# Performance work log

Measured on AMD Instinct MI355X. Metric: run time of the kernel, lower is better.

## Reference

```python
import jax, jax.numpy as jnp
import numpy as np

B, T, C = 8, 1024, 1024
NH, HD = 16, 64          # num_heads, head_dim (C = NH*HD)
NL = 8                   # num_layers
TPB = 64                 # tokens_per_block (block_causal)
EPS = 1e-5


def setup_inputs() -> dict:
    key = jax.random.key(0)
    ks = jax.random.split(key, 12)
    s = 0.02
    sequences = jax.random.normal(ks[0], (B, T, C), dtype=jnp.float32)
    # block-causal mask: causal OR same-block (tril | block_diag)
    idx = jnp.arange(T)
    mask = (idx[:, None] >= idx[None, :]) | ((idx[:, None] // TPB) == (idx[None, :] // TPB))
    # stacked per-layer params; torch Linear convention: W has shape [out, in]
    d = {
        "sequences": sequences,
        "mask": mask,
        "Wq": jax.random.normal(ks[1], (NL, C, C)) * s, "bq": jnp.zeros((NL, C)),
        "Wk": jax.random.normal(ks[2], (NL, C, C)) * s, "bk": jnp.zeros((NL, C)),
        "Wv": jax.random.normal(ks[3], (NL, C, C)) * s, "bv": jnp.zeros((NL, C)),
        "Wo": jax.random.normal(ks[4], (NL, C, C)) * s, "bo": jnp.zeros((NL, C)),
        "ln1w": jnp.ones((NL, C)), "ln1b": jnp.zeros((NL, C)),
        "ln2w": jnp.ones((NL, C)), "ln2b": jnp.zeros((NL, C)),
        "W1": jax.random.normal(ks[5], (NL, 4 * C, C)) * s, "b1": jnp.zeros((NL, 4 * C)),
        "W2": jax.random.normal(ks[6], (NL, C, 4 * C)) * s, "b2": jnp.zeros((NL, C)),
        "lnfw": jnp.ones((C,)), "lnfb": jnp.zeros((C,)),
    }
    return d


def _layernorm(x, w, b):
    m = jnp.mean(x, axis=-1, keepdims=True)
    v = jnp.mean(jnp.square(x - m), axis=-1, keepdims=True)
    return (x - m) * jax.lax.rsqrt(v + EPS) * w + b


def _linear(x, W, b):  # x: [..., in], W: [out, in]
    return jnp.einsum('...i,oi->...o', x, W) + b


def _attention(h, mask, Wq, bq, Wk, bk, Wv, bv, Wo, bo):
    # h: [B,T,C]
    q = _linear(h, Wq, bq).reshape(B, T, NH, HD)
    k = _linear(h, Wk, bk).reshape(B, T, NH, HD)
    v = _linear(h, Wv, bv).reshape(B, T, NH, HD)
    att = jnp.einsum('bqhd,bkhd->bhqk', q, k) * (HD ** -0.5)
    att = jnp.where(mask, att, -jnp.inf)
    att = jax.nn.softmax(att, axis=-1)
    y = jnp.einsum('bhqk,bkhd->bqhd', att, v).reshape(B, T, C)
    return _linear(y, Wo, bo)


def reference(sequences, mask, Wq, bq, Wk, bk, Wv, bv, Wo, bo,
              ln1w, ln1b, ln2w, ln2b, W1, b1, W2, b2, lnfw, lnfb):
    x = sequences  # dropout p=0
    for i in range(NL):
        h = _layernorm(x, ln1w[i], ln1b[i])
        x = x + _attention(h, mask, Wq[i], bq[i], Wk[i], bk[i], Wv[i], bv[i], Wo[i], bo[i])
        h = _layernorm(x, ln2w[i], ln2b[i])
        h = _linear(h, W1[i], b1[i])
        h = jax.nn.gelu(h, approximate=False)  # torch nn.GELU default = exact erf
        x = x + _linear(h, W2[i], b2[i])
    return _layernorm(x, lnfw, lnfb)
```

## Files before the change

### kernel.cpp

```cpp
#include <hip/hip_runtime.h>
#include <math.h>

typedef unsigned short ushort_t;
typedef __attribute__((ext_vector_type(4))) float f32x4;
typedef __attribute__((ext_vector_type(8))) short short8;

constexpr int BATCH = 8, T = 1024, C = 1024, NH = 16, HD = 64, NL = 8;
constexpr int MROWS = BATCH * T;
constexpr int CS = 3 * C;

#define WAITVM(n) asm volatile("s_waitcnt vmcnt(" #n ")" ::: "memory")
#define WAITLGKM0 asm volatile("s_waitcnt lgkmcnt(0)" ::: "memory")

__device__ __forceinline__ ushort_t f2bf(float f) {
  unsigned u = __builtin_bit_cast(unsigned, f);
  u += 0x7fffu + ((u >> 16) & 1u);
  return (ushort_t)(u >> 16);
}

__device__ __forceinline__ void gload_lds16(const ushort_t* g, ushort_t* l) {
  __builtin_amdgcn_global_load_lds(
      (const __attribute__((address_space(1))) unsigned int*)g,
      (__attribute__((address_space(3))) unsigned int*)l, 16, 0, 0);
}

__global__ __launch_bounds__(256, 8)
void convw_kernel(const float* __restrict__ Wq, const float* __restrict__ Wk,
                  const float* __restrict__ Wv, const float* __restrict__ Wo,
                  const float* __restrict__ W1, const float* __restrict__ W2,
                  const float* __restrict__ bq, const float* __restrict__ bk,
                  const float* __restrict__ bv,
                  ushort_t* __restrict__ wqkv, ushort_t* __restrict__ wo,
                  ushort_t* __restrict__ w1, ushort_t* __restrict__ w2,
                  float* __restrict__ bqkv)
{
  if (blockIdx.x == 6144) {
    int t = threadIdx.x;
    if (t < 384) {
      const float* s = (t < 128) ? (bq + t * 8)
                     : (t < 256) ? (bk + (t - 128) * 8)
                                 : (bv + (t - 256) * 8);
      f32x4 a = ((const f32x4*)s)[0], b = ((const f32x4*)s)[1];
      ((f32x4*)(bqkv + t * 8))[0] = a;
      ((f32x4*)(bqkv + t * 8))[1] = b;
    }
    return;
  }
  int g = blockIdx.x * 256 + threadIdx.x;
  const float* src;
  ushort_t* dst;
  if (g < 393216) {
    int which = g >> 17;
    int r = g & 131071;
    src = (which == 0 ? Wq : which == 1 ? Wk : Wv) + (size_t)r * 8;
    dst = wqkv + (size_t)g * 8;
  } else if (g < 524288) {
    int r = g - 393216;
    src = Wo + (size_t)r * 8; dst = wo + (size_t)r * 8;
  } else if (g < 1048576) {
    int r = g - 524288;
    src = W1 + (size_t)r * 8; dst = w1 + (size_t)r * 8;
  } else {
    int r = g - 1048576;
    src = W2 + (size_t)r * 8; dst = w2 + (size_t)r * 8;
  }
  f32x4 a = ((const f32x4*)src)[0], b = ((const f32x4*)src)[1];
  short8 o;
#pragma unroll
  for (int e = 0; e < 4; ++e) { o[e] = (short)f2bf(a[e]); o[e + 4] = (short)f2bf(b[e]); }
  *(short8*)dst = o;
}

template<int MODE>
__global__ __launch_bounds__(256, 4)
void gemm97(const ushort_t* __restrict__ A, const ushort_t* __restrict__ Wb,
            const float* __restrict__ bias, ushort_t* __restrict__ outb,
            float* __restrict__ resid, int K, int N, int nbn)
{
  __shared__ __align__(16) ushort_t Sm[2 * 128 * 64];
  ushort_t* As = Sm;
  ushort_t* Bs = Sm + 128 * 64;

  const int tid = threadIdx.x;
  const int lane = tid & 63, wave = tid >> 6;
  const int wm = wave >> 1, wn = wave & 1;
  const int l15 = lane & 15, l4 = lane >> 4;

  const int xcd = blockIdx.x & 7;
  const int local = blockIdx.x >> 3;
  const int grp = local >> 5, rem = local & 31;
  const int bm = xcd * 8 + (rem >> 2);
  const int bn = grp * 4 + (rem & 3);
  const long bm0 = (long)bm * 128;
  const long bn0 = (long)bn * 128;

  const ushort_t* srcA[4]; const ushort_t* srcB[4]; int dst4[4];
#pragma unroll
  for (int j = 0; j < 4; ++j) {
    int cidx = j * 256 + tid;
    int row = cidx >> 3;
    int cl = (cidx & 7) ^ (row & 7);
    srcA[j] = A + (size_t)(bm0 + row) * K + cl * 8;
    srcB[j] = Wb + (size_t)(bn0 + row) * K + cl * 8;
    dst4[j] = cidx * 8;
  }
  int aoff[2][4], boff[2][4];
#pragma unroll
  for (int ks = 0; ks < 2; ++ks) {
#pragma unroll
    for (int i = 0; i < 4; ++i) {
      int ra = wm * 64 + i * 16 + l15;
      aoff[ks][i] = ra * 64 + (((ks * 4 + l4) ^ (ra & 7)) << 3);
      int rb = wn * 64 + i * 16 + l15;
      boff[ks][i] = rb * 64 + (((ks * 4 + l4) ^ (rb & 7)) << 3);
    }
  }

  f32x4 acc[4][4] = {};
  const int nt = K >> 6;

  for (int t = 0; t < nt; ++t) {
    __syncthreads();
    const int kt = t << 6;
#pragma unroll
    for (int j = 0; j < 4; ++j) {
      gload_lds16(srcA[j] + kt, &As[dst4[j]]);
      gload_lds16(srcB[j] + kt, &Bs[dst4[j]]);
    }
    __syncthreads();
#pragma unroll
    for (int ks = 0; ks < 2; ++ks) {
      short8 af[4], bfr[4];
#pragma unroll
      for (int i = 0; i < 4; ++i) {
        af[i] = *(const short8*)&As[aoff[ks][i]];
        bfr[i] = *(const short8*)&Bs[boff[ks][i]];
      }
#pragma unroll
      for (int mi = 0; mi < 4; ++mi)
#pragma unroll
        for (int ni = 0; ni < 4; ++ni)
          acc[mi][ni] = __builtin_amdgcn_mfma_f32_16x16x32_bf16(
              af[mi], bfr[ni], acc[mi][ni], 0, 0, 0);
    }
  }
  __syncthreads();

  float* fl = (float*)Sm + wave * (16 * 68);
  const long grow0 = bm0 + wm * 64;
  const long gcol0 = bn0 + wn * 64;
  const int c8 = lane & 7;
  const f32x4 bb0 = *(const f32x4*)&bias[gcol0 + c8 * 8];
  const f32x4 bb1 = *(const f32x4*)&bias[gcol0 + c8 * 8 + 4];

#pragma unroll
  for (int mi = 0; mi < 4; ++mi) {
#pragma unroll
    for (int ni = 0; ni < 4; ++ni)
#pragma unroll
      for (int r = 0; r < 4; ++r)
        fl[(l4 * 4 + r) * 68 + ni * 16 + l15] = acc[mi][ni][r];
#pragma unroll
    for (int pass = 0; pass < 2; ++pass) {
      int row = pass * 8 + (lane >> 3);
      f32x4 v0 = *(const f32x4*)&fl[row * 68 + c8 * 8];
      f32x4 v1 = *(const f32x4*)&fl[row * 68 + c8 * 8 + 4];
      v0 += bb0; v1 += bb1;
      const long grow = grow0 + mi * 16 + row;
      if (MODE == 1) {
#pragma unroll
        for (int e = 0; e < 4; ++e) {
          v0[e] = 0.5f * v0[e] * (1.0f + erff(v0[e] * 0.70710678118f));
          v1[e] = 0.5f * v1[e] * (1.0f + erff(v1[e] * 0.70710678118f));
        }
      }
      if (MODE == 2) {
        float* rp = resid + (size_t)grow * N + gcol0 + c8 * 8;
        f32x4 r0 = *(const f32x4*)rp;
        f32x4 r1 = *(const f32x4*)(rp + 4);
        r0 += v0; r1 += v1;
        *(f32x4*)rp = r0;
        *(f32x4*)(rp + 4) = r1;
      } else {
        short8 o;
#pragma unroll
        for (int e = 0; e < 4; ++e) { o[e] = (short)f2bf(v0[e]); o[e + 4] = (short)f2bf(v1[e]); }
        *(short8*)&outb[(size_t)grow * N + gcol0 + c8 * 8] = o;
      }
    }
  }
}

__global__ __launch_bounds__(256, 4)
void attn_kernel(const ushort_t* __restrict__ qkv, ushort_t* __restrict__ y)
{
  __shared__ __align__(16) ushort_t Ks[2][64 * 64];
  __shared__ __align__(16) ushort_t Vts[2][64 * 64];
  __shared__ __align__(16) ushort_t Ps[64 * 64];
  const int tid = threadIdx.x;
  const int lane = tid & 63, wave = tid >> 6;
  const int l15 = lane & 15, l4 = lane >> 4;
  const int w16 = wave * 16;
  const int bh = blockIdx.x & 127, qpair = blockIdx.x >> 7;
  const int h = bh & 15, b = bh >> 4;
  const int qoff = h * HD, koff = C + h * HD, voff = 2 * C + h * HD;
  const int kvr = tid & 63, dc = tid >> 6;

#pragma unroll
  for (int half = 0; half < 2; ++half) {
    const int qb = half == 0 ? qpair : 15 - qpair;
    const int nkv = qb + 1;
    const size_t qrow0 = (size_t)(b * T + qb * 64);

    short8 aq[2];
#pragma unroll
    for (int ks = 0; ks < 2; ++ks)
      aq[ks] = *(const short8*)(qkv + (qrow0 + w16 + l15) * CS + qoff + ks * 32 + l4 * 8);

    f32x4 o[4] = {};
    float mrun[4] = {-INFINITY, -INFINITY, -INFINITY, -INFINITY};
    float lrun[4] = {0.f, 0.f, 0.f, 0.f};

    {
      const size_t krow0 = (size_t)(b * T);
#pragma unroll
      for (int j = 0; j < 2; ++j) {
        int cidx = j * 256 + tid;
        int row = cidx >> 3, cl = (cidx & 7) ^ (row & 7);
        gload_lds16(qkv + (krow0 + row) * CS + koff + cl * 8, &Ks[0][cidx * 8]);
      }
    }
    short8 vreg0, vreg1;
    vreg0 = *(const short8*)(qkv + ((size_t)(b * T) + kvr) * CS + voff + dc * 8);
    vreg1 = *(const short8*)(qkv + ((size_t)(b * T) + kvr) * CS + voff + (dc + 4) * 8);
    WAITVM(2);
    __builtin_amdgcn_s_barrier();

    for (int t = 0; t < nkv; ++t) {
      const int buf = t & 1;
      const bool more = (t + 1 < nkv);
      short8 vnext0, vnext1;
      if (more) {
        const size_t krow1 = (size_t)(b * T + (t + 1) * 64);
#pragma unroll
        for (int j = 0; j < 2; ++j) {
          int cidx = j * 256 + tid;
          int row = cidx >> 3, cl = (cidx & 7) ^ (row & 7);
          gload_lds16(qkv + (krow1 + row) * CS + koff + cl * 8, &Ks[buf ^ 1][cidx * 8]);
        }
        vnext0 = *(const short8*)(qkv + (krow1 + kvr) * CS + voff + dc * 8);
        vnext1 = *(const short8*)(qkv + (krow1 + kvr) * CS + voff + (dc + 4) * 8);
      }

      f32x4 s[4] = {};
#pragma unroll
      for (int ks = 0; ks < 2; ++ks) {
#pragma unroll
        for (int n = 0; n < 4; ++n) {
          int br = n * 16 + l15;
          int pb = (ks * 4 + l4) ^ (br & 7);
          short8 bk2 = *(const short8*)&Ks[buf][br * 64 + pb * 8];
          s[n] = __builtin_amdgcn_mfma_f32_16x16x32_bf16(aq[ks], bk2, s[n], 0, 0, 0);
        }
      }

#pragma unroll
      for (int r = 0; r < 4; ++r) {
        float mx = fmaxf(fmaxf(s[0][r], s[1][r]), fmaxf(s[2][r], s[3][r]));
#pragma unroll
        for (int d = 1; d < 16; d <<= 1) mx = fmaxf(mx, __shfl_xor(mx, d, 16));
        mx *= 0.125f;
        float mnew = fmaxf(mrun[r], mx);
        float alpha = __expf(mrun[r] - mnew);
        float rowsum = 0.f;
        int qr = w16 + l4 * 4 + r;
#pragma unroll
        for (int n = 0; n < 4; ++n) {
          float pv = __expf(s[n][r] * 0.125f - mnew);
          rowsum += pv;
          int kv = n * 16 + l15;
          Ps[qr * 64 + (((kv >> 3) ^ (qr & 7)) << 3) + (kv & 7)] = f2bf(pv);
        }
#pragma unroll
        for (int d = 1; d < 16; d <<= 1) rowsum += __shfl_xor(rowsum, d, 16);
        mrun[r] = mnew;
        lrun[r] = lrun[r] * alpha + rowsum;
        o[0][r] *= alpha; o[1][r] *= alpha; o[2][r] *= alpha; o[3][r] *= alpha;
      }

#pragma unroll
      for (int i = 0; i < 8; ++i) {
        int d0 = dc * 8 + i;
        Vts[buf][d0 * 64 + (((kvr >> 3) ^ (d0 & 7)) << 3) + (kvr & 7)] = (ushort_t)vreg0[i];
        int d1 = (dc + 4) * 8 + i;
        Vts[buf][d1 * 64 + (((kvr >> 3) ^ (d1 & 7)) << 3) + (kvr & 7)] = (ushort_t)vreg1[i];
      }
      vreg0 = vnext0; vreg1 = vnext1;

      WAITLGKM0;
      __builtin_amdgcn_s_barrier();

#pragma unroll
      for (int ks = 0; ks < 2; ++ks) {
        int arow = w16 + l15;
        int pa = (ks * 4 + l4) ^ (arow & 7);
        short8 ap = *(const short8*)&Ps[arow * 64 + pa * 8];
#pragma unroll
        for (int n = 0; n < 4; ++n) {
          int vr = n * 16 + l15;
          int pb = (ks * 4 + l4) ^ (vr & 7);
          short8 bvv = *(const short8*)&Vts[buf][vr * 64 + pb * 8];
          o[n] = __builtin_amdgcn_mfma_f32_16x16x32_bf16(ap, bvv, o[n], 0, 0, 0);
        }
      }

      if (more) { WAITVM(2); }
      __builtin_amdgcn_s_barrier();
    }

#pragma unroll
    for (int n = 0; n < 4; ++n) {
#pragma unroll
      for (int r = 0; r < 4; ++r) {
        float val = o[n][r] / lrun[r];
        y[(qrow0 + w16 + l4 * 4 + r) * C + h * HD + n * 16 + l15] = f2bf(val);
      }
    }
    __builtin_amdgcn_s_barrier();
  }
}

template<int OUTBF16>
__global__ __launch_bounds__(256, 4)
void ln_kernel(const float* __restrict__ x, const float* __restrict__ w,
               const float* __restrict__ bprm, void* __restrict__ out)
{
  const size_t row = blockIdx.x;
  const int tid = threadIdx.x;
  f32x4 xv = ((const f32x4*)(x + row * 1024))[tid];
  float s1 = xv[0] + xv[1] + xv[2] + xv[3];
  float s2 = xv[0] * xv[0] + xv[1] * xv[1] + xv[2] * xv[2] + xv[3] * xv[3];
#pragma unroll
  for (int m = 1; m < 64; m <<= 1) {
    s1 += __shfl_xor(s1, m);
    s2 += __shfl_xor(s2, m);
  }
  __shared__ float red[8];
  const int wave = tid >> 6, lane = tid & 63;
  if (lane == 0) { red[wave * 2] = s1; red[wave * 2 + 1] = s2; }
  __syncthreads();
  s1 = red[0] + red[2] + red[4] + red[6];
  s2 = red[1] + red[3] + red[5] + red[7];
  const float mean = s1 * (1.f / 1024.f);
  const float var = s2 * (1.f / 1024.f) - mean * mean;
  const float rstd = rsqrtf(var + 1e-5f);
  f32x4 wv = ((const f32x4*)w)[tid];
  f32x4 bv = ((const f32x4*)bprm)[tid];
  f32x4 ov;
#pragma unroll
  for (int c2 = 0; c2 < 4; ++c2) ov[c2] = (xv[c2] - mean) * rstd * wv[c2] + bv[c2];
  if (OUTBF16) {
    ushort4 u;
    u.x = f2bf(ov[0]); u.y = f2bf(ov[1]); u.z = f2bf(ov[2]); u.w = f2bf(ov[3]);
    ((ushort4*)out)[row * 256 + tid] = u;
  } else {
    ((f32x4*)out)[row * 256 + tid] = ov;
  }
}

extern "C" void kernel_launch(void* const* d_in, const int* in_sizes, int n_in,
                              void* d_out, int out_size, void* d_ws, size_t ws_size,
                              hipStream_t stream)
{
  const float* seq  = (const float*)d_in[0];
  const float* Wq   = (const float*)d_in[2];  const float* bq = (const float*)d_in[3];
  const float* Wk   = (const float*)d_in[4];  const float* bk = (const float*)d_in[5];
  const float* Wv   = (const float*)d_in[6];  const float* bv = (const float*)d_in[7];
  const float* Wo   = (const float*)d_in[8];  const float* bo = (const float*)d_in[9];
  const float* ln1w = (const float*)d_in[10]; const float* ln1b = (const float*)d_in[11];
  const float* ln2w = (const float*)d_in[12]; const float* ln2b = (const float*)d_in[13];
  const float* W1   = (const float*)d_in[14]; const float* b1 = (const float*)d_in[15];
  const float* W2   = (const float*)d_in[16]; const float* b2 = (const float*)d_in[17];
  const float* lnfw = (const float*)d_in[18]; const float* lnfb = (const float*)d_in[19];

  char* ws = (char*)d_ws;
  size_t off = 0;
  float* X = (float*)(ws + off);         off += (size_t)MROWS * C * 4;
  ushort_t* Hb = (ushort_t*)(ws + off);  off += (size_t)MROWS * C * 2;
  ushort_t* Yb = (ushort_t*)(ws + off);  off += (size_t)MROWS * C * 2;
  ushort_t* BIG = (ushort_t*)(ws + off); off += (size_t)MROWS * 4 * C * 2;
  ushort_t* wqkv = (ushort_t*)(ws + off); off += (size_t)3 * C * C * 2;
  ushort_t* wo   = (ushort_t*)(ws + off); off += (size_t)C * C * 2;
  ushort_t* w1   = (ushort_t*)(ws + off); off += (size_t)4 * C * C * 2;
  ushort_t* w2   = (ushort_t*)(ws + off); off += (size_t)4 * C * C * 2;
  float* bqkv = (float*)(ws + off);       off += (size_t)3 * C * 4;
  ushort_t* QKVb = BIG;
  ushort_t* Gb = BIG;

  hipMemcpyAsync(X, seq, (size_t)MROWS * C * 4, hipMemcpyDeviceToDevice, stream);

  const dim3 blk(256);
  const dim3 gQKV(1536);
  const dim3 gWo(512);
  const dim3 gW1(2048);
  const dim3 gW2(512);
  const dim3 gAttn(1024);
  const dim3 gConv(6145);

  for (int i = 0; i < NL; ++i) {
    const size_t w1Off = (size_t)i * C * C;
    const size_t w4Off = (size_t)i * 4 * C * C;
    convw_kernel<<<gConv, blk, 0, stream>>>(Wq + w1Off, Wk + w1Off, Wv + w1Off,
                                            Wo + w1Off, W1 + w4Off, W2 + w4Off,
                                            bq + i * C, bk + i * C, bv + i * C,
                                            wqkv, wo, w1, w2, bqkv);
    ln_kernel<1><<<MROWS, blk, 0, stream>>>(X, ln1w + i * C, ln1b + i * C, Hb);
    gemm97<0><<<gQKV, blk, 0, stream>>>(Hb, wqkv, bqkv, QKVb, nullptr, C, CS, 24);
    attn_kernel<<<gAttn, blk, 0, stream>>>(QKVb, Yb);
    gemm97<2><<<gWo, blk, 0, stream>>>(Yb, wo, bo + i * C, nullptr, X, C, C, 8);
    ln_kernel<1><<<MROWS, blk, 0, stream>>>(X, ln2w + i * C, ln2b + i * C, Hb);
    gemm97<1><<<gW1, blk, 0, stream>>>(Hb, w1, b1 + (size_t)i * 4 * C, Gb, nullptr, C, 4 * C, 32);
    gemm97<2><<<gW2, blk, 0, stream>>>(Gb, w2, b2 + i * C, nullptr, X, 4 * C, C, 8);
  }
  ln_kernel<0><<<MROWS, blk, 0, stream>>>(X, lnfw, lnfb, (float*)d_out);
}
```

Before: 2.829 ms.

## Add 8-wave large-tile GEMM kernel for MLP projections

Adds a new 512-thread GEMM kernel using 256x256 (W1) and 128x256 (W2) output tiles, with a four-phase ping-pong schedule that interleaves LDS fragment reads, async global-to-LDS loads of the next K-tile halves, and MFMA bursts under raised wave priority. It also remaps block indices so that each XCD handles a contiguous M range. The MLP up and down projections switch to this kernel with fewer, larger blocks, aiming for more data reuse per block and better overlap of loads with compute. The trade-offs are one block per CU, higher register and LDS pressure, and fewer blocks for the W2 launch (256), which may leave some CUs idle.

Result: slower. 3.209 ms (+13.4%).

```diff
diff --git a/kernel.cpp b/kernel.cpp
--- a/kernel.cpp
+++ b/kernel.cpp
@@ -191,6 +191,229 @@
   }
 }
 
+template<int MODE, int BM>
+__global__ __launch_bounds__(512, 1)
+void gemm8(const ushort_t* __restrict__ A, const ushort_t* __restrict__ Wb,
+           const float* __restrict__ bias, ushort_t* __restrict__ outb,
+           float* __restrict__ resid, int K, int N, int nbn)
+{
+  constexpr int MI = BM / 32;
+  constexpr int MIH = MI / 2;
+  constexpr int LA = BM / 128;
+  constexpr int AH = (BM / 2) * 64;
+  constexpr int BH = 128 * 64;
+
+  __shared__ __align__(16) ushort_t As[2][2 * AH];
+  __shared__ __align__(16) ushort_t Bs[2][2 * BH];
+
+  const int tid = threadIdx.x;
+  const int lane = tid & 63, wave = tid >> 6;
+  const int wm = wave >> 2, wn = wave & 3;
+  const int l15 = lane & 15, l4 = lane >> 4;
+
+  const int xcd = blockIdx.x & 7;
+  const int local = blockIdx.x >> 3;
+  const int bmt = (8192 / BM) / 8;
+  const int bm = xcd * bmt + local / nbn;
+  const int bn = local % nbn;
+  const long bm0 = (long)bm * BM;
+  const long bn0 = (long)bn * 256;
+
+  const ushort_t* srcA[2][LA];
+#pragma unroll
+  for (int h = 0; h < 2; ++h)
+#pragma unroll
+    for (int j = 0; j < LA; ++j) {
+      int cidx = j * 512 + tid;
+      int rowL = cidx >> 3, c = cidx & 7;
+      int cl = c ^ (rowL & 7);
+      srcA[h][j] = A + (size_t)(bm0 + h * (BM / 2) + rowL) * K + cl * 8;
+    }
+  const ushort_t* srcB[2][2];
+#pragma unroll
+  for (int h = 0; h < 2; ++h)
+#pragma unroll
+    for (int j = 0; j < 2; ++j) {
+      int cidx = j * 512 + tid;
+      int rowL = cidx >> 3, c = cidx & 7;
+      int cl = c ^ (rowL & 7);
+      srcB[h][j] = Wb + (size_t)(bn0 + h * 128 + rowL) * K + cl * 8;
+    }
+
+  auto stageA = [&](int tau, int h) {
+#pragma unroll
+    for (int j = 0; j < LA; ++j) {
+      int cidx = j * 512 + tid;
+      gload_lds16(srcA[h][j] + (tau << 6), &As[tau & 1][h * AH + cidx * 8]);
+    }
+  };
+  auto stageB = [&](int tau, int h) {
+#pragma unroll
+    for (int j = 0; j < 2; ++j) {
+      int cidx = j * 512 + tid;
+      gload_lds16(srcB[h][j] + (tau << 6), &Bs[tau & 1][h * BH + cidx * 8]);
+    }
+  };
+
+  int aoffs[2][MI], boffs[2][4];
+#pragma unroll
+  for (int ks = 0; ks < 2; ++ks) {
+#pragma unroll
+    for (int mi = 0; mi < MI; ++mi) {
+      int mh = mi / MIH, mo = mi % MIH;
+      int rowL = wm * (BM / 4) + mo * 16 + l15;
+      aoffs[ks][mi] = mh * AH + rowL * 64 + (((ks * 4 + l4) ^ (rowL & 7)) << 3);
+    }
+#pragma unroll
+    for (int ni = 0; ni < 4; ++ni) {
+      int nh = ni >> 1, no = ni & 1;
+      int rowL = wn * 32 + no * 16 + l15;
+      boffs[ks][ni] = nh * BH + rowL * 64 + (((ks * 4 + l4) ^ (rowL & 7)) << 3);
+    }
+  }
+
+  f32x4 acc[MI][4] = {};
+  const int nt = K >> 6;
+
+  stageA(0, 0); stageB(0, 0); stageA(0, 1); stageB(0, 1);
+  stageA(1, 0); stageB(1, 0);
+  if constexpr (BM == 256) WAITVM(4); else WAITVM(3);
+  __builtin_amdgcn_s_barrier();
+
+  for (int t = 0; t < nt; ++t) {
+    const int buf = t & 1;
+    short8 af[2][MIH], bfr[2][2];
+
+#pragma unroll
+    for (int k2 = 0; k2 < 2; ++k2) {
+#pragma unroll
+      for (int mo = 0; mo < MIH; ++mo) af[k2][mo] = *(const short8*)&As[buf][aoffs[k2][mo]];
+#pragma unroll
+      for (int no = 0; no < 2; ++no) bfr[k2][no] = *(const short8*)&Bs[buf][boffs[k2][no]];
+    }
+    if (t + 1 < nt) stageA(t + 1, 1);
+    __builtin_amdgcn_s_barrier();
+    __builtin_amdgcn_s_setprio(1);
+#pragma unroll
+    for (int k2 = 0; k2 < 2; ++k2)
+#pragma unroll
+      for (int mo = 0; mo < MIH; ++mo)
+#pragma unroll
+        for (int no = 0; no < 2; ++no)
+          acc[mo][no] = __builtin_amdgcn_mfma_f32_16x16x32_bf16(
+              af[k2][mo], bfr[k2][no], acc[mo][no], 0, 0, 0);
+    __builtin_amdgcn_s_setprio(0);
+    __builtin_amdgcn_s_barrier();
+
+#pragma unroll
+    for (int k2 = 0; k2 < 2; ++k2)
+#pragma unroll
+      for (int no = 0; no < 2; ++no) bfr[k2][no] = *(const short8*)&Bs[buf][boffs[k2][2 + no]];
+    if (t + 1 < nt) stageB(t + 1, 1);
+    __builtin_amdgcn_s_barrier();
+    __builtin_amdgcn_s_setprio(1);
+#pragma unroll
+    for (int k2 = 0; k2 < 2; ++k2)
+#pragma unroll
+      for (int mo = 0; mo < MIH; ++mo)
+#pragma unroll
+        for (int no = 0; no < 2; ++no)
+          acc[mo][2 + no] = __builtin_amdgcn_mfma_f32_16x16x32_bf16(
+              af[k2][mo], bfr[k2][no], acc[mo][2 + no], 0, 0, 0);
+    __builtin_amdgcn_s_setprio(0);
+    __builtin_amdgcn_s_barrier();
+
+#pragma unroll
+    for (int k2 = 0; k2 < 2; ++k2) {
+#pragma unroll
+      for (int mo = 0; mo < MIH; ++mo) af[k2][mo] = *(const short8*)&As[buf][aoffs[k2][MIH + mo]];
+#pragma unroll
+      for (int no = 0; no < 2; ++no) bfr[k2][no] = *(const short8*)&Bs[buf][boffs[k2][no]];
+    }
+    if (t + 2 < nt) stageA(t + 2, 0);
+    __builtin_amdgcn_s_barrier();
+    __builtin_amdgcn_s_setprio(1);
+#pragma unroll
+    for (int k2 = 0; k2 < 2; ++k2)
+#pragma unroll
+      for (int mo = 0; mo < MIH; ++mo)
+#pragma unroll
+        for (int no = 0; no < 2; ++no)
+          acc[MIH + mo][no] = __builtin_amdgcn_mfma_f32_16x16x32_bf16(
+              af[k2][mo], bfr[k2][no], acc[MIH + mo][no], 0, 0, 0);
+    __builtin_amdgcn_s_setprio(0);
+    __builtin_amdgcn_s_barrier();
+
+#pragma unroll
+    for (int k2 = 0; k2 < 2; ++k2)
+#pragma unroll
+      for (int no = 0; no < 2; ++no) bfr[k2][no] = *(const short8*)&Bs[buf][boffs[k2][2 + no]];
+    if (t + 2 < nt) stageB(t + 2, 0);
+    if (t < nt - 2) { if constexpr (BM == 256) WAITVM(4); else WAITVM(3); }
+    else if (t == nt - 2) { WAITVM(0); }
+    __builtin_amdgcn_s_barrier();
+    __builtin_amdgcn_s_setprio(1);
+#pragma unroll
+    for (int k2 = 0; k2 < 2; ++k2)
+#pragma unroll
+      for (int mo = 0; mo < MIH; ++mo)
+#pragma unroll
+        for (int no = 0; no < 2; ++no)
+          acc[MIH + mo][2 + no] = __builtin_amdgcn_mfma_f32_16x16x32_bf16(
+              af[k2][mo], bfr[k2][no], acc[MIH + mo][2 + no], 0, 0, 0);
+    __builtin_amdgcn_s_setprio(0);
+    __builtin_amdgcn_s_barrier();
+  }
+  __syncthreads();
+
+  float* fl = (float*)&Bs[0][0] + wave * (16 * 68);
+  const int c8 = lane & 7;
+  const long gcol = bn0 + ((c8 < 4) ? (wn * 32 + c8 * 8) : (128 + wn * 32 + (c8 - 4) * 8));
+  const f32x4 bb0 = *(const f32x4*)&bias[gcol];
+  const f32x4 bb1 = *(const f32x4*)&bias[gcol + 4];
+
+#pragma unroll
+  for (int mi = 0; mi < MI; ++mi) {
+    const long rowBase = bm0 + (mi >= MIH ? BM / 2 : 0) + wm * (BM / 4) + (mi % MIH) * 16;
+#pragma unroll
+    for (int ni = 0; ni < 4; ++ni)
+#pragma unroll
+      for (int r = 0; r < 4; ++r)
+        fl[(l4 * 4 + r) * 68 + ni * 16 + l15] = acc[mi][ni][r];
+    __builtin_amdgcn_s_barrier();
+#pragma unroll
+    for (int pass = 0; pass < 2; ++pass) {
+      int row = pass * 8 + (lane >> 3);
+      int tcol = (c8 < 4) ? (c8 * 8) : (32 + (c8 - 4) * 8);
+      f32x4 v0 = *(const f32x4*)&fl[row * 68 + tcol];
+      f32x4 v1 = *(const f32x4*)&fl[row * 68 + tcol + 4];
+      v0 += bb0; v1 += bb1;
+      const long grow = rowBase + row;
+      if (MODE == 1) {
+#pragma unroll
+        for (int e = 0; e < 4; ++e) {
+          v0[e] = 0.5f * v0[e] * (1.0f + erff(v0[e] * 0.70710678118f));
+          v1[e] = 0.5f * v1[e] * (1.0f + erff(v1[e] * 0.70710678118f));
+        }
+      }
+      if (MODE == 2) {
+        float* rp = resid + (size_t)grow * N + gcol;
+        f32x4 r0 = *(const f32x4*)rp;
+        f32x4 r1 = *(const f32x4*)(rp + 4);
+        r0 += v0; r1 += v1;
+        *(f32x4*)rp = r0;
+        *(f32x4*)(rp + 4) = r1;
+      } else {
+        short8 o;
+#pragma unroll
+        for (int e = 0; e < 4; ++e) { o[e] = (short)f2bf(v0[e]); o[e + 4] = (short)f2bf(v1[e]); }
+        *(short8*)&outb[(size_t)grow * N + gcol] = o;
+      }
+    }
+    __builtin_amdgcn_s_barrier();
+  }
+}
+
 __global__ __launch_bounds__(256, 4)
 void attn_kernel(const ushort_t* __restrict__ qkv, ushort_t* __restrict__ y)
 {
@@ -400,10 +623,11 @@
   hipMemcpyAsync(X, seq, (size_t)MROWS * C * 4, hipMemcpyDeviceToDevice, stream);
 
   const dim3 blk(256);
+  const dim3 blk512(512);
   const dim3 gQKV(1536);
   const dim3 gWo(512);
-  const dim3 gW1(2048);
-  const dim3 gW2(512);
+  const dim3 gW1(512);
+  const dim3 gW2(256);
   const dim3 gAttn(1024);
   const dim3 gConv(6145);
 
@@ -419,8 +643,8 @@
     attn_kernel<<<gAttn, blk, 0, stream>>>(QKVb, Yb);
     gemm97<2><<<gWo, blk, 0, stream>>>(Yb, wo, bo + i * C, nullptr, X, C, C, 8);
     ln_kernel<1><<<MROWS, blk, 0, stream>>>(X, ln2w + i * C, ln2b + i * C, Hb);
-    gemm97<1><<<gW1, blk, 0, stream>>>(Hb, w1, b1 + (size_t)i * 4 * C, Gb, nullptr, C, 4 * C, 32);
-    gemm97<2><<<gW2, blk, 0, stream>>>(Gb, w2, b2 + i * C, nullptr, X, 4 * C, C, 8);
+    gemm8<1, 256><<<gW1, blk512, 0, stream>>>(Hb, w1, b1 + (size_t)i * 4 * C, Gb, nullptr, C, 4 * C, 16);
+    gemm8<2, 128><<<gW2, blk512, 0, stream>>>(Gb, w2, b2 + i * C, nullptr, X, 4 * C, C, 4);
   }
   ln_kernel<0><<<MROWS, blk, 0, stream>>>(X, lnfw, lnfb, (float*)d_out);
 }
```
